# Optimization experiments

Measured on AMD Instinct MI355X. Metric: run time of the kernel, lower is better.

Reference implementation:

```python
import jax, jax.numpy as jnp
import numpy as np

E = 2048      # embed_dim
HQ = 32       # num_query_heads
HKV = 8       # num_kv_heads
DH = E // HQ  # head_dim = 64
G = HQ // HKV # group_size = 4
KV_DIM = E * HKV // HQ  # 512
B, S = 2, 2048


def setup_inputs() -> dict:
    key = jax.random.key(0)
    ks = jax.random.split(key, 11)
    sc_in = 1.0 / np.sqrt(E)
    sc_attn = 1.0 / np.sqrt(E)
    return {
        "query": jax.random.normal(ks[0], (B, S, E), jnp.float32),
        "key": jax.random.normal(ks[1], (B, S, E), jnp.float32),
        "value": jax.random.normal(ks[2], (B, S, E), jnp.float32),
        "Wq": jax.random.normal(ks[3], (E, E), jnp.float32) * sc_in,
        "bq": jnp.zeros((E,), jnp.float32),
        "Wk": jax.random.normal(ks[4], (E, KV_DIM), jnp.float32) * sc_in,
        "bk": jnp.zeros((KV_DIM,), jnp.float32),
        "Wv": jax.random.normal(ks[5], (E, KV_DIM), jnp.float32) * sc_in,
        "bv": jnp.zeros((KV_DIM,), jnp.float32),
        "Wo": jax.random.normal(ks[6], (E, E), jnp.float32) * sc_attn,
        "bo": jnp.zeros((E,), jnp.float32),
    }


def reference(query, key, value, Wq, bq, Wk, bk, Wv, bv, Wo, bo):
    b, s, _ = query.shape
    # projections
    Q = (query @ Wq + bq).reshape(b, s, HQ, DH).transpose(0, 2, 1, 3)   # [B,HQ,S,DH]
    K = (key @ Wk + bk).reshape(b, s, HKV, DH).transpose(0, 2, 1, 3)    # [B,HKV,S,DH]
    V = (value @ Wv + bv).reshape(b, s, HKV, DH).transpose(0, 2, 1, 3)  # [B,HKV,S,DH]
    # GQA: repeat_interleave along head dim (kv head h -> query heads h*G..h*G+G-1)
    K = jnp.repeat(K, G, axis=1)  # [B,HQ,S,DH]
    V = jnp.repeat(V, G, axis=1)  # [B,HQ,S,DH]
    scores = jnp.einsum('bhqd,bhkd->bhqk', Q, K) / np.sqrt(DH).astype(np.float32)
    attn_weights = jax.nn.softmax(scores, axis=-1)                      # [B,HQ,S,S]
    attn_out = jnp.einsum('bhqk,bhkd->bhqd', attn_weights, V)           # [B,HQ,S,DH]
    attn_out = attn_out.transpose(0, 2, 1, 3).reshape(b, s, E)
    out = attn_out @ Wo + bo
    return out, attn_weights
```

## Files before the change

### kernel.cpp

```cpp
#include <hip/hip_runtime.h>
#include <stdint.h>

typedef _Float16 f16;
typedef _Float16 f16x8 __attribute__((ext_vector_type(8)));
typedef _Float16 f16x4 __attribute__((ext_vector_type(4)));
typedef float    f32x4 __attribute__((ext_vector_type(4)));

#define SEQ   2048
#define EDIM  2048
#define NHQ   32
#define NHKV  8
#define DHEAD 64
#define KVD   512
#define NB    2
#define NTOK  (NB*SEQ)
#define QKVN  3072
#define SCALE 0.1803368801111204f

__device__ __forceinline__ f32x4 mfma16(f16x8 a, f16x8 b, f32x4 c) {
  return __builtin_amdgcn_mfma_f32_16x16x32_f16(a, b, c, 0, 0, 0);
}

__device__ __forceinline__ void gload_lds16(const void* g, void* l) {
  __builtin_amdgcn_global_load_lds(
      (const __attribute__((address_space(1))) void*)g,
      (__attribute__((address_space(3))) void*)l, 16, 0, 0);
}

__global__ __launch_bounds__(256) void k_prep(
    const float* __restrict__ q, const float* __restrict__ k,
    const float* __restrict__ v, f16* __restrict__ d3,
    const float* __restrict__ Wq, const float* __restrict__ Wo,
    f16* __restrict__ wqT, f16* __restrict__ woT,
    const float* __restrict__ Wk, const float* __restrict__ Wv,
    f16* __restrict__ wkT, f16* __restrict__ wvT)
{
  __shared__ float t[32][33];
  const int blk = blockIdx.x;
  if (blk < 24576) {
    int i = blk * 256 + threadIdx.x;
    int tt = i >> 21, j = i & ((1 << 21) - 1);
    const float* s = tt == 0 ? q : (tt == 1 ? k : v);
    float4 vv = reinterpret_cast<const float4*>(s)[j];
    f16x4 h;
    h[0] = (f16)vv.x; h[1] = (f16)vv.y; h[2] = (f16)vv.z; h[3] = (f16)vv.w;
    reinterpret_cast<f16x4*>(d3)[i] = h;
    return;
  }
  const float* s; f16* d; int C, tr, tc;
  if (blk < 32768) {
    int bb = blk - 24576;
    int z = bb >> 12; bb &= 4095;
    tr = bb >> 6; tc = bb & 63;
    s = z ? Wo : Wq; d = z ? woT : wqT; C = EDIM;
  } else {
    int bb = blk - 32768;
    int z = bb >> 10; bb &= 1023;
    tr = bb >> 4; tc = bb & 15;
    s = z ? Wv : Wk; d = z ? wvT : wkT; C = KVD;
  }
  int lr = threadIdx.x >> 3, lc = (threadIdx.x & 7) << 2;
  float4 vv = *reinterpret_cast<const float4*>(&s[(size_t)(tr*32+lr)*C + tc*32 + lc]);
  t[lr][lc+0] = vv.x; t[lr][lc+1] = vv.y; t[lr][lc+2] = vv.z; t[lr][lc+3] = vv.w;
  __syncthreads();
  f16x4 h;
  h[0] = (f16)t[lc+0][lr];
  h[1] = (f16)t[lc+1][lr];
  h[2] = (f16)t[lc+2][lr];
  h[3] = (f16)t[lc+3][lr];
  *reinterpret_cast<f16x4*>(&d[(size_t)(tc*32+lr)*EDIM + tr*32 + lc]) = h;
}

__global__ __launch_bounds__(256) void k_trv(const f16* __restrict__ qkv,
                                             f16* __restrict__ dst) {
  __shared__ f16 t[64][68];
  int bh = blockIdx.x;
  int st = blockIdx.y;
  int b = bh >> 3, h = bh & 7;
  #pragma unroll
  for (int i = 0; i < 4; ++i) {
    int sl = i*16 + (threadIdx.x >> 4);
    int d4 = (threadIdx.x & 15) * 4;
    *(f16x4*)&t[sl][d4] =
        *(const f16x4*)&qkv[(size_t)(b*SEQ + st*64 + sl)*QKVN + 2560 + h*DHEAD + d4];
  }
  __syncthreads();
  #pragma unroll
  for (int i = 0; i < 4; ++i) {
    int dl = i*16 + (threadIdx.x >> 4);
    int s4 = (threadIdx.x & 15) * 4;
    f16x4 v;
    v[0] = t[s4+0][dl]; v[1] = t[s4+1][dl]; v[2] = t[s4+2][dl]; v[3] = t[s4+3][dl];
    *(f16x4*)&dst[(size_t)(bh*DHEAD + dl)*SEQ + st*64 + s4] = v;
  }
}

__global__ __launch_bounds__(256) void k_gemm_qkv(
    const f16* __restrict__ Abase,
    const f16* __restrict__ Wt,
    const float* __restrict__ bq, const float* __restrict__ bk,
    const float* __restrict__ bv,
    f16* __restrict__ Cout)
{
  const int flat = blockIdx.y * gridDim.x + blockIdx.x;
  const int xcd = flat & 7, idx = flat >> 3;
  const int tn = xcd*3 + (idx % 3);
  const int tm = idx / 3;
  const int sel = (tn >= 16) + (tn >= 20);
  const f16* A = Abase + (size_t)sel*NTOK*EDIM;
  const float* bias = sel == 0 ? bq : (sel == 1 ? bk : bv);
  const int coff = sel == 0 ? 0 : (sel == 1 ? 2048 : 2560);

  __shared__ f16 sA[128*64];
  __shared__ f16 sB[128*64];
  const int tid  = threadIdx.x;
  const int lane = tid & 63, wv = tid >> 6;
  const int wm = wv >> 1, wn = wv & 1;
  const int l15 = lane & 15, lhi = lane >> 4;

  const f32x4 zz = {0.f, 0.f, 0.f, 0.f};
  f32x4 acc[4][4];
  #pragma unroll
  for (int m = 0; m < 4; ++m)
    #pragma unroll
    for (int n = 0; n < 4; ++n) acc[m][n] = zz;

  const f16* gsrc[8];
  f16* ldst[8];
  #pragma unroll
  for (int i = 0; i < 8; ++i) {
    int u = wv*8 + i;
    int r  = (u & 15)*8 + (lane >> 3);
    int cb = ((lane & 7) << 4) ^ ((r & 7) << 4);
    if (u < 16) {
      gsrc[i] = A  + (size_t)(tm*128 + r)*EDIM + (cb >> 1);
      ldst[i] = sA + u*512;
    } else {
      gsrc[i] = Wt + (size_t)(tn*128 + r)*EDIM + (cb >> 1);
      ldst[i] = sB + (u - 16)*512;
    }
  }

  int aoff[2][4], boff[2][4];
  #pragma unroll
  for (int ks = 0; ks < 2; ++ks)
    #pragma unroll
    for (int m = 0; m < 4; ++m) {
      int ra = wm*64 + m*16 + l15;
      aoff[ks][m] = ra*128 + ((ks*64 + (lhi << 4)) ^ ((ra & 7) << 4));
      int rb = wn*64 + m*16 + l15;
      boff[ks][m] = rb*128 + ((ks*64 + (lhi << 4)) ^ ((rb & 7) << 4));
    }

  for (int kb = 0; kb < EDIM/64; ++kb) {
    #pragma unroll
    for (int i = 0; i < 8; ++i)
      gload_lds16(gsrc[i] + kb*64, ldst[i]);
    __syncthreads();
    #pragma unroll
    for (int ks = 0; ks < 2; ++ks) {
      f16x8 af[4], bf[4];
      #pragma unroll
      for (int m = 0; m < 4; ++m)
        af[m] = *(const f16x8*)((const char*)sA + aoff[ks][m]);
      #pragma unroll
      for (int n = 0; n < 4; ++n)
        bf[n] = *(const f16x8*)((const char*)sB + boff[ks][n]);
      #pragma unroll
      for (int m = 0; m < 4; ++m)
        #pragma unroll
        for (int n = 0; n < 4; ++n)
          acc[m][n] = mfma16(af[m], bf[n], acc[m][n]);
    }
    __syncthreads();
  }

  float bcol[4];
  #pragma unroll
  for (int n = 0; n < 4; ++n)
    bcol[n] = bias[tn*128 + wn*64 + n*16 + l15 - coff];
  #pragma unroll
  for (int m = 0; m < 4; ++m)
    #pragma unroll
    for (int n = 0; n < 4; ++n)
      #pragma unroll
      for (int r = 0; r < 4; ++r) {
        int row = tm*128 + wm*64 + m*16 + lhi*4 + r;
        int col = tn*128 + wn*64 + n*16 + l15;
        Cout[(size_t)row*QKVN + col] = (f16)(acc[m][n][r] + bcol[n]);
      }
}

__global__ __launch_bounds__(256) void k_gemm(
    const f16* __restrict__ A, const f16* __restrict__ Bt,
    const float* __restrict__ bias, float* __restrict__ Cout,
    int M, int N, int K)
{
  const int flat = blockIdx.y * gridDim.x + blockIdx.x;
  const int xcd = flat & 7, idx = flat >> 3;
  const int tn = xcd*2 + (idx & 1);
  const int tm = idx >> 1;

  __shared__ f16 sA[128*64];
  __shared__ f16 sB[128*64];
  const int tid  = threadIdx.x;
  const int lane = tid & 63, wv = tid >> 6;
  const int wm = wv >> 1, wn = wv & 1;
  const int l15 = lane & 15, lhi = lane >> 4;

  const f32x4 zz = {0.f, 0.f, 0.f, 0.f};
  f32x4 acc[4][4];
  #pragma unroll
  for (int m = 0; m < 4; ++m)
    #pragma unroll
    for (int n = 0; n < 4; ++n) acc[m][n] = zz;

  const f16* gsrc[8];
  f16* ldst[8];
  #pragma unroll
  for (int i = 0; i < 8; ++i) {
    int u = wv*8 + i;
    int r  = (u & 15)*8 + (lane >> 3);
    int cb = ((lane & 7) << 4) ^ ((r & 7) << 4);
    if (u < 16) {
      gsrc[i] = A  + (size_t)(tm*128 + r)*K + (cb >> 1);
      ldst[i] = sA + u*512;
    } else {
      gsrc[i] = Bt + (size_t)(tn*128 + r)*K + (cb >> 1);
      ldst[i] = sB + (u - 16)*512;
    }
  }

  int aoff[2][4], boff[2][4];
  #pragma unroll
  for (int ks = 0; ks < 2; ++ks)
    #pragma unroll
    for (int m = 0; m < 4; ++m) {
      int ra = wm*64 + m*16 + l15;
      aoff[ks][m] = ra*128 + ((ks*64 + (lhi << 4)) ^ ((ra & 7) << 4));
      int rb = wn*64 + m*16 + l15;
      boff[ks][m] = rb*128 + ((ks*64 + (lhi << 4)) ^ ((rb & 7) << 4));
    }

  const int nkb = K >> 6;
  for (int kb = 0; kb < nkb; ++kb) {
    #pragma unroll
    for (int i = 0; i < 8; ++i)
      gload_lds16(gsrc[i] + kb*64, ldst[i]);
    __syncthreads();
    #pragma unroll
    for (int ks = 0; ks < 2; ++ks) {
      f16x8 af[4], bf[4];
      #pragma unroll
      for (int m = 0; m < 4; ++m)
        af[m] = *(const f16x8*)((const char*)sA + aoff[ks][m]);
      #pragma unroll
      for (int n = 0; n < 4; ++n)
        bf[n] = *(const f16x8*)((const char*)sB + boff[ks][n]);
      #pragma unroll
      for (int m = 0; m < 4; ++m)
        #pragma unroll
        for (int n = 0; n < 4; ++n)
          acc[m][n] = mfma16(af[m], bf[n], acc[m][n]);
    }
    __syncthreads();
  }

  float bcol[4];
  #pragma unroll
  for (int n = 0; n < 4; ++n)
    bcol[n] = bias[tn*128 + wn*64 + n*16 + l15];
  #pragma unroll
  for (int m = 0; m < 4; ++m)
    #pragma unroll
    for (int n = 0; n < 4; ++n)
      #pragma unroll
      for (int r = 0; r < 4; ++r) {
        int row = tm*128 + wm*64 + m*16 + lhi*4 + r;
        int col = tn*128 + wn*64 + n*16 + l15;
        __builtin_nontemporal_store(acc[m][n][r] + bcol[n],
                                    &Cout[(size_t)row*N + col]);
      }
}

__global__ __launch_bounds__(256) void k_attn(
    const f16* __restrict__ QKV,
    const f16* __restrict__ Vt,
    float* __restrict__ wout,
    f16* __restrict__ AO)
{
  __shared__ f16 sK[2][64*64];
  __shared__ f16 sV[2][64*64];
  __shared__ f16 sW[4][16*64];
  const int tid = threadIdx.x, lane = tid & 63, wv = tid >> 6;
  const int bid = (blockIdx.x & 7) * 256 + (blockIdx.x >> 3);
  const int b = bid >> 10, h = (bid >> 5) & 31, qb = bid & 31;
  const int hk = h >> 2;
  const int l15 = lane & 15, lhi = lane >> 4;
  const int rloc = (lane >> 3) & 7, chk = lane & 7;
  const int csw = (chk ^ rloc) * 8;
  const int sw  = (l15 & 7) << 4;
  const int qrow0 = qb*64 + wv*16;
  const f32x4 zz = {0.f, 0.f, 0.f, 0.f};

  f16x8 qf[2];
  #pragma unroll
  for (int ks = 0; ks < 2; ++ks)
    qf[ks] = *(const f16x8*)&QKV[(size_t)(b*SEQ + qrow0 + l15)*QKVN
                                 + h*DHEAD + ks*32 + lhi*8];

  const f16* Kb = QKV + 2048 + (size_t)(b*SEQ)*QKVN + hk*DHEAD;
  const f16* Vb = Vt + (size_t)((b*NHKV + hk)*DHEAD)*SEQ;

  float lsum = 0.f;
  {
    #pragma unroll
    for (int i = 0; i < 2; ++i) {
      int u = wv*2 + i;
      gload_lds16(Kb + (size_t)(u*8 + rloc)*QKVN + csw, &sK[0][u*512]);
    }
    __syncthreads();
    int buf = 0;
    for (int kb = 0; kb < SEQ/64; ++kb) {
      if (kb < SEQ/64 - 1) {
        #pragma unroll
        for (int i = 0; i < 2; ++i) {
          int u = wv*2 + i;
          gload_lds16(Kb + (size_t)((kb+1)*64 + u*8 + rloc)*QKVN + csw, &sK[buf^1][u*512]);
        }
      }
      #pragma unroll
      for (int kt = 0; kt < 4; ++kt) {
        const char* kbase = (const char*)&sK[buf][0] + (kt*16 + l15)*128;
        f16x8 kf0 = *(const f16x8*)(kbase + ((lhi*16) ^ sw));
        f16x8 kf1 = *(const f16x8*)(kbase + ((64 + lhi*16) ^ sw));
        __builtin_amdgcn_s_setprio(1);
        f32x4 s = zz;
        s = mfma16(kf0, qf[0], s);
        s = mfma16(kf1, qf[1], s);
        __builtin_amdgcn_s_setprio(0);
        #pragma unroll
        for (int r = 0; r < 4; ++r)
          lsum += __builtin_amdgcn_exp2f(s[r] * SCALE);
      }
      __syncthreads();
      buf ^= 1;
    }
  }
  float den = lsum;
  den += __shfl_xor(den, 16);
  den += __shfl_xor(den, 32);
  const float nldr = -__builtin_amdgcn_logf(den);

  f32x4 o[4];
  #pragma unroll
  for (int dt = 0; dt < 4; ++dt) o[dt] = zz;

  f16* swv = &sW[wv][0];
  float* wrow = wout + (size_t)((b*NHQ + h)*SEQ + qrow0)*SEQ;

  {
    #pragma unroll
    for (int i = 0; i < 2; ++i) {
      int u = wv*2 + i;
      gload_lds16(Kb + (size_t)(u*8 + rloc)*QKVN + csw, &sK[0][u*512]);
      gload_lds16(Vb + (size_t)(u*8 + rloc)*SEQ + csw, &sV[0][u*512]);
    }
    __syncthreads();
    int buf = 0;
    for (int kb = 0; kb < SEQ/64; ++kb) {
      if (kb < SEQ/64 - 1) {
        #pragma unroll
        for (int i = 0; i < 2; ++i) {
          int u = wv*2 + i;
          gload_lds16(Kb + (size_t)((kb+1)*64 + u*8 + rloc)*QKVN + csw, &sK[buf^1][u*512]);
          gload_lds16(Vb + (size_t)(u*8 + rloc)*SEQ + (kb+1)*64 + csw, &sV[buf^1][u*512]);
        }
      }
      __builtin_amdgcn_sched_barrier(0);
      #pragma unroll
      for (int kt = 0; kt < 4; ++kt) {
        const char* kbase = (const char*)&sK[buf][0] + (kt*16 + l15)*128;
        f16x8 kf0 = *(const f16x8*)(kbase + ((lhi*16) ^ sw));
        f16x8 kf1 = *(const f16x8*)(kbase + ((64 + lhi*16) ^ sw));
        __builtin_amdgcn_s_setprio(1);
        f32x4 s = zz;
        s = mfma16(kf0, qf[0], s);
        s = mfma16(kf1, qf[1], s);
        __builtin_amdgcn_s_setprio(0);
        f32x4 wvec;
        f16x4 wh;
        #pragma unroll
        for (int r = 0; r < 4; ++r) {
          float wgt = __builtin_amdgcn_exp2f(__builtin_fmaf(s[r], SCALE, nldr));
          wvec[r] = wgt;
          wh[r] = (f16)wgt;
        }
        __builtin_nontemporal_store(wvec,
            (f32x4*)(wrow + (size_t)l15*SEQ + kb*64 + kt*16 + lhi*4));
        *(f16x4*)((char*)swv + l15*128 + ((kt*32 + lhi*8) ^ sw)) = wh;
      }
      __builtin_amdgcn_s_setprio(1);
      #pragma unroll
      for (int ks = 0; ks < 2; ++ks) {
        f16x8 af = *(const f16x8*)((const char*)swv + l15*128 + ((ks*64 + lhi*16) ^ sw));
        #pragma unroll
        for (int dt = 0; dt < 4; ++dt) {
          const char* vbase = (const char*)&sV[buf][0] + (dt*16 + l15)*128;
          f16x8 vf = *(const f16x8*)(vbase + ((ks*64 + lhi*16) ^ sw));
          o[dt] = mfma16(af, vf, o[dt]);
        }
      }
      __builtin_amdgcn_s_setprio(0);
      asm volatile("s_waitcnt vmcnt(4)" ::: "memory");
      __builtin_amdgcn_s_barrier();
      __builtin_amdgcn_sched_barrier(0);
      buf ^= 1;
    }
  }

  #pragma unroll
  for (int dt = 0; dt < 4; ++dt)
    #pragma unroll
    for (int r = 0; r < 4; ++r)
      AO[(size_t)(b*SEQ + qrow0 + lhi*4 + r)*EDIM + h*DHEAD + dt*16 + l15]
          = (f16)o[dt][r];
}

extern "C" void kernel_launch(void* const* d_in, const int* in_sizes, int n_in,
                              void* d_out, int out_size, void* d_ws, size_t ws_size,
                              hipStream_t stream) {
  (void)in_sizes; (void)n_in; (void)out_size; (void)ws_size;
  const float* query = (const float*)d_in[0];
  const float* key   = (const float*)d_in[1];
  const float* value = (const float*)d_in[2];
  const float* Wq    = (const float*)d_in[3];
  const float* bq    = (const float*)d_in[4];
  const float* Wk    = (const float*)d_in[5];
  const float* bk    = (const float*)d_in[6];
  const float* Wv    = (const float*)d_in[7];
  const float* bv    = (const float*)d_in[8];
  const float* Wo    = (const float*)d_in[9];
  const float* bo    = (const float*)d_in[10];

  float* out   = (float*)d_out;
  float* wattn = out + (size_t)NTOK*EDIM;

  f16* p    = (f16*)d_ws;
  f16* q16  = p;  p += (size_t)NTOK*EDIM;
  f16* k16  = p;  p += (size_t)NTOK*EDIM;
  f16* v16  = p;  p += (size_t)NTOK*EDIM;
  f16* wqT  = p;  p += (size_t)EDIM*EDIM;
  f16* wkT  = p;  p += (size_t)KVD*EDIM;
  f16* wvT  = p;  p += (size_t)KVD*EDIM;
  f16* woT  = p;  p += (size_t)EDIM*EDIM;
  f16* QKVp = p;  p += (size_t)NTOK*QKVN;
  f16* Vt   = p;  p += (size_t)NTOK*KVD;
  f16* AO   = p;  p += (size_t)NTOK*EDIM;
  (void)k16; (void)v16;

  k_prep<<<34816, 256, 0, stream>>>(query, key, value, q16,
                                    Wq, Wo, wqT, woT, Wk, Wv, wkT, wvT);

  k_gemm_qkv<<<dim3(QKVN/128, NTOK/128), 256, 0, stream>>>(
      q16, wqT, bq, bk, bv, QKVp);

  k_trv<<<dim3(NB*NHKV, SEQ/64), 256, 0, stream>>>(QKVp, Vt);

  k_attn<<<NB*NHQ*(SEQ/64), 256, 0, stream>>>(QKVp, Vt, wattn, AO);

  k_gemm<<<dim3(EDIM/128, NTOK/128), 256, 0, stream>>>(
      AO, woT, bo, out, NTOK, EDIM, EDIM);
}
```

Before: 476.9 us.

## Split softmax denominator pass into separate kernel fused with V transpose

Moves the first pass of attention, which computes the per-row log-sum-exp denominator, out of the attention kernel into a new kernel that also handles the V transpose blocks, and passes the result through a global buffer. The attention kernel then only runs the second pass, lowering its register and LDS pressure and shortening each block. In exchange there is an extra global round trip for the denominators. The same work is still done, only scheduled across two launches instead of one.

After: 526.9 us. +10.5%, slower.

```diff
diff --git a/kernel.cpp b/kernel.cpp
--- a/kernel.cpp
+++ b/kernel.cpp
@@ -71,30 +71,6 @@
   *reinterpret_cast<f16x4*>(&d[(size_t)(tc*32+lr)*EDIM + tr*32 + lc]) = h;
 }
 
-__global__ __launch_bounds__(256) void k_trv(const f16* __restrict__ qkv,
-                                             f16* __restrict__ dst) {
-  __shared__ f16 t[64][68];
-  int bh = blockIdx.x;
-  int st = blockIdx.y;
-  int b = bh >> 3, h = bh & 7;
-  #pragma unroll
-  for (int i = 0; i < 4; ++i) {
-    int sl = i*16 + (threadIdx.x >> 4);
-    int d4 = (threadIdx.x & 15) * 4;
-    *(f16x4*)&t[sl][d4] =
-        *(const f16x4*)&qkv[(size_t)(b*SEQ + st*64 + sl)*QKVN + 2560 + h*DHEAD + d4];
-  }
-  __syncthreads();
-  #pragma unroll
-  for (int i = 0; i < 4; ++i) {
-    int dl = i*16 + (threadIdx.x >> 4);
-    int s4 = (threadIdx.x & 15) * 4;
-    f16x4 v;
-    v[0] = t[s4+0][dl]; v[1] = t[s4+1][dl]; v[2] = t[s4+2][dl]; v[3] = t[s4+3][dl];
-    *(f16x4*)&dst[(size_t)(bh*DHEAD + dl)*SEQ + st*64 + s4] = v;
-  }
-}
-
 __global__ __launch_bounds__(256) void k_gemm_qkv(
     const f16* __restrict__ Abase,
     const f16* __restrict__ Wt,
@@ -283,9 +259,100 @@
       }
 }
 
+__global__ __launch_bounds__(256) void k_dentrv(
+    const f16* __restrict__ QKV,
+    f16* __restrict__ Vt,
+    float* __restrict__ nld)
+{
+  __shared__ f16 sK[2][64*64];
+  __shared__ f16 t[64][68];
+  if (blockIdx.x >= 2048) {
+    int idx = blockIdx.x - 2048;
+    int bh = idx & 15, st = idx >> 4;
+    int b = bh >> 3, h = bh & 7;
+    #pragma unroll
+    for (int i = 0; i < 4; ++i) {
+      int sl = i*16 + (threadIdx.x >> 4);
+      int d4 = (threadIdx.x & 15) * 4;
+      *(f16x4*)&t[sl][d4] =
+          *(const f16x4*)&QKV[(size_t)(b*SEQ + st*64 + sl)*QKVN + 2560 + h*DHEAD + d4];
+    }
+    __syncthreads();
+    #pragma unroll
+    for (int i = 0; i < 4; ++i) {
+      int dl = i*16 + (threadIdx.x >> 4);
+      int s4 = (threadIdx.x & 15) * 4;
+      f16x4 v;
+      v[0] = t[s4+0][dl]; v[1] = t[s4+1][dl]; v[2] = t[s4+2][dl]; v[3] = t[s4+3][dl];
+      *(f16x4*)&Vt[(size_t)(bh*DHEAD + dl)*SEQ + st*64 + s4] = v;
+    }
+    return;
+  }
+  const int tid = threadIdx.x, lane = tid & 63, wv = tid >> 6;
+  const int bid = (blockIdx.x & 7) * 256 + (blockIdx.x >> 3);
+  const int b = bid >> 10, h = (bid >> 5) & 31, qb = bid & 31;
+  const int hk = h >> 2;
+  const int l15 = lane & 15, lhi = lane >> 4;
+  const int rloc = (lane >> 3) & 7, chk = lane & 7;
+  const int csw = (chk ^ rloc) * 8;
+  const int sw  = (l15 & 7) << 4;
+  const int qrow0 = qb*64 + wv*16;
+  const f32x4 zz = {0.f, 0.f, 0.f, 0.f};
+
+  f16x8 qf[2];
+  #pragma unroll
+  for (int ks = 0; ks < 2; ++ks)
+    qf[ks] = *(const f16x8*)&QKV[(size_t)(b*SEQ + qrow0 + l15)*QKVN
+                                 + h*DHEAD + ks*32 + lhi*8];
+
+  const f16* Kb = QKV + 2048 + (size_t)(b*SEQ)*QKVN + hk*DHEAD;
+
+  float lsum = 0.f;
+  {
+    #pragma unroll
+    for (int i = 0; i < 2; ++i) {
+      int u = wv*2 + i;
+      gload_lds16(Kb + (size_t)(u*8 + rloc)*QKVN + csw, &sK[0][u*512]);
+    }
+    __syncthreads();
+    int buf = 0;
+    for (int kb = 0; kb < SEQ/64; ++kb) {
+      if (kb < SEQ/64 - 1) {
+        #pragma unroll
+        for (int i = 0; i < 2; ++i) {
+          int u = wv*2 + i;
+          gload_lds16(Kb + (size_t)((kb+1)*64 + u*8 + rloc)*QKVN + csw, &sK[buf^1][u*512]);
+        }
+      }
+      #pragma unroll
+      for (int kt = 0; kt < 4; ++kt) {
+        const char* kbase = (const char*)&sK[buf][0] + (kt*16 + l15)*128;
+        f16x8 kf0 = *(const f16x8*)(kbase + ((lhi*16) ^ sw));
+        f16x8 kf1 = *(const f16x8*)(kbase + ((64 + lhi*16) ^ sw));
+        __builtin_amdgcn_s_setprio(1);
+        f32x4 s = zz;
+        s = mfma16(kf0, qf[0], s);
+        s = mfma16(kf1, qf[1], s);
+        __builtin_amdgcn_s_setprio(0);
+        #pragma unroll
+        for (int r = 0; r < 4; ++r)
+          lsum += __builtin_amdgcn_exp2f(s[r] * SCALE);
+      }
+      __syncthreads();
+      buf ^= 1;
+    }
+  }
+  float den = lsum;
+  den += __shfl_xor(den, 16);
+  den += __shfl_xor(den, 32);
+  if (lane < 16)
+    nld[(size_t)(b*NHQ + h)*SEQ + qrow0 + lane] = -__builtin_amdgcn_logf(den);
+}
+
 __global__ __launch_bounds__(256) void k_attn(
     const f16* __restrict__ QKV,
     const f16* __restrict__ Vt,
+    const float* __restrict__ nld,
     float* __restrict__ wout,
     f16* __restrict__ AO)
 {
@@ -311,46 +378,7 @@
 
   const f16* Kb = QKV + 2048 + (size_t)(b*SEQ)*QKVN + hk*DHEAD;
   const f16* Vb = Vt + (size_t)((b*NHKV + hk)*DHEAD)*SEQ;
-
-  float lsum = 0.f;
-  {
-    #pragma unroll
-    for (int i = 0; i < 2; ++i) {
-      int u = wv*2 + i;
-      gload_lds16(Kb + (size_t)(u*8 + rloc)*QKVN + csw, &sK[0][u*512]);
-    }
-    __syncthreads();
-    int buf = 0;
-    for (int kb = 0; kb < SEQ/64; ++kb) {
-      if (kb < SEQ/64 - 1) {
-        #pragma unroll
-        for (int i = 0; i < 2; ++i) {
-          int u = wv*2 + i;
-          gload_lds16(Kb + (size_t)((kb+1)*64 + u*8 + rloc)*QKVN + csw, &sK[buf^1][u*512]);
-        }
-      }
-      #pragma unroll
-      for (int kt = 0; kt < 4; ++kt) {
-        const char* kbase = (const char*)&sK[buf][0] + (kt*16 + l15)*128;
-        f16x8 kf0 = *(const f16x8*)(kbase + ((lhi*16) ^ sw));
-        f16x8 kf1 = *(const f16x8*)(kbase + ((64 + lhi*16) ^ sw));
-        __builtin_amdgcn_s_setprio(1);
-        f32x4 s = zz;
-        s = mfma16(kf0, qf[0], s);
-        s = mfma16(kf1, qf[1], s);
-        __builtin_amdgcn_s_setprio(0);
-        #pragma unroll
-        for (int r = 0; r < 4; ++r)
-          lsum += __builtin_amdgcn_exp2f(s[r] * SCALE);
-      }
-      __syncthreads();
-      buf ^= 1;
-    }
-  }
-  float den = lsum;
-  den += __shfl_xor(den, 16);
-  den += __shfl_xor(den, 32);
-  const float nldr = -__builtin_amdgcn_logf(den);
+  const float nldr = nld[(size_t)(b*NHQ + h)*SEQ + qrow0 + l15];
 
   f32x4 o[4];
   #pragma unroll
@@ -457,6 +485,7 @@
   f16* QKVp = p;  p += (size_t)NTOK*QKVN;
   f16* Vt   = p;  p += (size_t)NTOK*KVD;
   f16* AO   = p;  p += (size_t)NTOK*EDIM;
+  float* nld = (float*)p;
   (void)k16; (void)v16;
 
   k_prep<<<34816, 256, 0, stream>>>(query, key, value, q16,
@@ -465,9 +494,9 @@
   k_gemm_qkv<<<dim3(QKVN/128, NTOK/128), 256, 0, stream>>>(
       q16, wqT, bq, bk, bv, QKVp);
 
-  k_trv<<<dim3(NB*NHKV, SEQ/64), 256, 0, stream>>>(QKVp, Vt);
-
-  k_attn<<<NB*NHQ*(SEQ/64), 256, 0, stream>>>(QKVp, Vt, wattn, AO);
+  k_dentrv<<<2560, 256, 0, stream>>>(QKVp, Vt, nld);
+
+  k_attn<<<NB*NHQ*(SEQ/64), 256, 0, stream>>>(QKVp, Vt, nld, wattn, AO);
 
   k_gemm<<<dim3(EDIM/128, NTOK/128), 256, 0, stream>>>(
       AO, woT, bo, out, NTOK, EDIM, EDIM);
```
